# Kernel optimization log

Measured on AMD Instinct MI355X. Metric: run time of the kernel, lower is better.

Reference implementation:

```python
import jax, jax.numpy as jnp
import numpy as np

N, G, MAX_N, E, H = 20000, 200, 100, 320000, 4
F_IN, NHID, NCLS = 128, 128, 10
DQ = 2 * NHID   # pooling-stack input dim = 2*nhid
K1 = 25         # ceil(0.25 * avg_num_nodes)


def _lin(key, fi, fo):
    kw, kb = jax.random.split(key)
    s = 1.0 / np.sqrt(fi)
    return (jax.random.uniform(kw, (fi, fo), jnp.float32, -s, s),
            jax.random.uniform(kb, (fo,), jnp.float32, -s, s))


def setup_inputs():
    key = jax.random.key(0)
    ks = jax.random.split(key, 32)
    x = jax.random.normal(ks[0], (N, F_IN), jnp.float32)
    gid = jax.random.randint(ks[1], (E,), 0, G)
    u = jax.random.randint(ks[2], (E,), 0, MAX_N)
    v = jax.random.randint(ks[3], (E,), 0, MAX_N)
    edge_index = jnp.stack([gid * MAX_N + u, gid * MAX_N + v]).astype(jnp.int32)
    batch = (jnp.arange(N) // MAX_N).astype(jnp.int32)
    d = {}
    d['x'], d['edge_index'], d['batch'] = x, edge_index, batch
    d['W1'], d['b1'] = _lin(ks[4], F_IN, NHID)
    d['W2'], d['b2'] = _lin(ks[5], NHID, NHID)
    d['S0'] = jax.random.normal(ks[6], (1, K1, DQ), jnp.float32) * (1.0 / np.sqrt(DQ))
    d['Wq0'], d['bq0'] = _lin(ks[7], DQ, DQ)
    d['Wk0'], d['bk0'] = _lin(ks[8], DQ, DQ)
    d['Wv0'], d['bv0'] = _lin(ks[9], DQ, DQ)
    d['Wo0'], d['bo0'] = _lin(ks[10], DQ, DQ)
    d['Wq1'], d['bq1'] = _lin(ks[11], DQ, NHID)
    d['Wk1'], d['bk1'] = _lin(ks[12], DQ, NHID)
    d['Wv1'], d['bv1'] = _lin(ks[13], DQ, NHID)
    d['Wo1'], d['bo1'] = _lin(ks[14], NHID, NHID)
    d['S2'] = jax.random.normal(ks[15], (1, 1, NHID), jnp.float32) * (1.0 / np.sqrt(NHID))
    d['Wq2'], d['bq2'] = _lin(ks[16], NHID, NHID)
    d['Wk2'], d['bk2'] = _lin(ks[17], NHID, NHID)
    d['Wv2'], d['bv2'] = _lin(ks[18], NHID, NHID)
    d['Wo2'], d['bo2'] = _lin(ks[19], NHID, NHID)
    d['Wl'], d['bl'] = _lin(ks[20], NHID, NHID)
    d['Wc1'], d['bc1'] = _lin(ks[21], NHID, NHID)
    d['Wc2'], d['bc2'] = _lin(ks[22], NHID, NHID // 2)
    d['Wc3'], d['bc3'] = _lin(ks[23], NHID // 2, NCLS)
    return d


def gcn(h, src, dst, W, b):
    # PyG GCNConv: add self loops, sym-normalize, scatter-add, bias
    h = h @ W
    loop = jnp.arange(N, dtype=src.dtype)
    s = jnp.concatenate([src, loop])
    t = jnp.concatenate([dst, loop])
    deg = jax.ops.segment_sum(jnp.ones(s.shape[0], h.dtype), t, num_segments=N)
    dinv = jax.lax.rsqrt(jnp.maximum(deg, 1.0))
    norm = (dinv[s] * dinv[t])[:, None]
    return jax.ops.segment_sum(h[s] * norm, t, num_segments=N) + b


def to_dense(v, batch):
    counts = jax.ops.segment_sum(jnp.ones(v.shape[0], jnp.int32), batch, num_segments=G)
    start = jnp.cumsum(counts) - counts
    pos = jnp.arange(v.shape[0]) - start[batch]
    dense = jnp.zeros((G, MAX_N, v.shape[1]), v.dtype).at[batch, pos].set(v)
    mask = jnp.zeros((G, MAX_N), bool).at[batch, pos].set(True)
    return dense, mask


def attn_block(Q, K, V, Wo, bo, mask_bias):
    # MAB core with cluster=True: softmax over the QUERY (seed) axis, ln=False
    B, nq, dv = Q.shape
    dh = dv // H
    Qh = Q.reshape(B, nq, H, dh)
    Kh = K.reshape(B, K.shape[1], H, dh)
    Vh = V.reshape(B, V.shape[1], H, dh)
    score = jnp.einsum('bqhd,bkhd->bhqk', Qh, Kh) / jnp.sqrt(jnp.float32(dv))
    if mask_bias is not None:
        score = score + mask_bias[:, None, None, :]
    A = jax.nn.softmax(score, axis=2)  # cluster assignment over seeds
    O = Q + jnp.einsum('bhqk,bkhd->bqhd', A, Vh).reshape(B, nq, dv)
    return O + jax.nn.relu(O @ Wo + bo)


def reference(x, edge_index, batch, W1, b1, W2, b2, S0, Wq0, bq0, Wk0, bk0, Wv0, bv0, Wo0, bo0,
              Wq1, bq1, Wk1, bk1, Wv1, bv1, Wo1, bo1, S2, Wq2, bq2, Wk2, bk2, Wv2, bv2, Wo2, bo2,
              Wl, bl, Wc1, bc1, Wc2, bc2, Wc3, bc3):
    src, dst = edge_index[0], edge_index[1]
    x1 = jax.nn.relu(gcn(x, src, dst, W1, b1))
    x2 = jax.nn.relu(gcn(x1, src, dst, W2, b2))
    p1 = jax.ops.segment_sum(x1, batch, num_segments=G)  # global_add_pool
    p2 = jax.ops.segment_sum(x2, batch, num_segments=G)
    xcat = jnp.concatenate([x1, x2], axis=1)             # [N, 2*nhid]
    dense, mask = to_dense(xcat, batch)
    mask_bias = (1.0 - mask.astype(jnp.float32)) * -1e9
    # --- GMPool_G: PMA with GCNConv for K/V on the node graph ---
    Kd, _ = to_dense(gcn(xcat, src, dst, Wk0, bk0), batch)
    Vd, _ = to_dense(gcn(xcat, src, dst, Wv0, bv0), batch)
    Q0 = jnp.broadcast_to(S0, (G, K1, DQ)) @ Wq0 + bq0
    O0 = attn_block(Q0, Kd, Vd, Wo0, bo0, mask_bias)     # [G, 25, 256]
    # --- SelfAtt (SAB), mask consumed above ---
    Q1 = O0 @ Wq1 + bq1
    K1d = O0 @ Wk1 + bk1
    V1d = O0 @ Wv1 + bv1
    O1 = attn_block(Q1, K1d, V1d, Wo1, bo1, None)        # [G, 25, 128]
    # --- GMPool_I: PMA with 1 seed ---
    Q2 = jnp.broadcast_to(S2, (G, 1, NHID)) @ Wq2 + bq2
    K2d = O1 @ Wk2 + bk2
    V2d = O1 @ Wv2 + bv2
    O2 = attn_block(Q2, K2d, V2d, Wo2, bo2, None)        # [G, 1, 128]
    z = (O2 @ Wl + bl)[:, 0, :]
    z = jax.nn.relu(z @ Wc1 + bc1)                        # dropout = identity at eval
    z = jax.nn.relu(z @ Wc2 + bc2)
    logits = z @ Wc3 + bc3
    return (logits, p1, p2)
```

## Files before the change

kernel.cpp:

```cpp
#include <hip/hip_runtime.h>
#include <hip/hip_bf16.h>
#include <cstdint>
#include <cstddef>

typedef __hip_bfloat16 bf16;
typedef __attribute__((ext_vector_type(8))) short s16x8;
typedef __attribute__((ext_vector_type(4))) float f32x4;

#define MAXN 100
#define HH   4
#define FIN  128
#define KS1  25
#define GLDK 136

static inline int ceil_div(int a, int b){ return (a + b - 1) / b; }

__device__ inline short f2bf(float f){
  unsigned int u = __float_as_uint(f);
  u = (u + 0x7FFF + ((u >> 16) & 1)) >> 16;
  return (short)u;
}
__device__ inline float loadf(const void* s, size_t i, bool isbf){
  return isbf ? __bfloat162float(((const bf16*)s)[i]) : ((const float*)s)[i];
}
__device__ inline bool block_sniff(const void* x, int tid, int* flagS){
  if (tid < 64){
    unsigned short b = ((const unsigned short*)x)[2 * tid];
    float v = __uint_as_float(((unsigned)b) << 16);
    float a = fabsf(v);
    bool ok = (a >= 6.1e-5f && a <= 16384.f);
    unsigned long long m = __ballot(ok);
    if (tid == 0) *flagS = (__popcll(m) >= 32) ? 1 : 0;
  }
  __syncthreads();
  return *flagS != 0;
}

struct PrepBatch {
  const void* src[40];
  void*       dst[40];
  int         a[40];
  int         b[40];
  int         blk0[41];
  int         ne;
  const void* xptr;
};

__global__ __launch_bounds__(256) void prep_all(PrepBatch pb){
  __shared__ int flagS;
  int tid = threadIdx.x;
  bool isbf = block_sniff(pb.xptr, tid, &flagS);
  int blk = blockIdx.x;
  int t = 0;
  while (t + 1 < pb.ne && pb.blk0[t + 1] <= blk) t++;
  int local = blk - pb.blk0[t];
  const void* s = pb.src[t];
  int bt = pb.b[t];
  if (bt < 0){
    float val = (bt == -2) ? 1.0f : 0.0f;
    int n = pb.a[t];
    float* d = (float*)pb.dst[t];
    int v = local * 256 + tid;
    int base = v * 4;
    if (base + 3 < n) ((float4*)d)[v] = make_float4(val, val, val, val);
    else for (int j = base; j < n && j < base + 4; j++) d[j] = val;
  } else if (bt == 0){
    int n = pb.a[t];
    float* d = (float*)pb.dst[t];
    int v = local * 256 + tid;
    int base = v * 4;
    if (base + 3 < n){
      float4 f;
      if (isbf){
        ushort4 u = ((const ushort4*)s)[v];
        f.x = __uint_as_float(((unsigned)u.x) << 16);
        f.y = __uint_as_float(((unsigned)u.y) << 16);
        f.z = __uint_as_float(((unsigned)u.z) << 16);
        f.w = __uint_as_float(((unsigned)u.w) << 16);
      } else f = ((const float4*)s)[v];
      ((float4*)d)[v] = f;
    } else {
      for (int j = base; j < n && j < base + 4; j++) d[j] = loadf(s, j, isbf);
    }
  } else {
    int K = pb.a[t], Nn = bt, ldt = K + 8;
    short* d = (short*)pb.dst[t];
    int i = local * 256 + tid;
    if (i < K * Nn){
      int n = i / K, k = i - n * K;
      d[(size_t)n * ldt + k] = f2bf(loadf(s, (size_t)k * Nn + n, isbf));
    }
  }
}

__global__ __launch_bounds__(256) void adj_cnt(const int* __restrict__ src, const int* __restrict__ dst,
                                               float* __restrict__ A, int e){
  int i = blockIdx.x * 256 + threadIdx.x;
  if (i >= e) return;
  int s = src[i], d = dst[i];
  int g = d / MAXN;
  int dl = d - g * MAXN;
  int sl = s - (s / MAXN) * MAXN;
  atomicAdd(&A[(size_t)g * (MAXN * MAXN) + dl * MAXN + sl], 1.0f);
}

__global__ __launch_bounds__(256) void ubar_q0(const float* __restrict__ S0,
    const float* __restrict__ Wq0, const float* __restrict__ bq0,
    const float* __restrict__ Wk0, const float* __restrict__ bk0,
    float* __restrict__ Q0, short* __restrict__ Ubart, float* __restrict__ cvec)
{
  __shared__ float q0s[64];
  int j = blockIdx.x, h = j / 25, q = j - h * 25;
  int tid = threadIdx.x;
  if (tid < 64){
    int c = h * 64 + tid;
    float acc = bq0[c];
    for (int e = 0; e < 256; e++) acc = fmaf(S0[q * 256 + e], Wq0[e * 256 + c], acc);
    q0s[tid] = acc;
    Q0[q * 256 + c] = acc;
  }
  __syncthreads();
  float acc = 0.f;
  const float* wp = &Wk0[(size_t)tid * 256 + h * 64];
#pragma unroll
  for (int d = 0; d < 64; d++) acc = fmaf(wp[d], q0s[d], acc);
  Ubart[(size_t)j * 264 + tid] = f2bf(acc * 0.0625f);
  if (tid == 0){
    float cb = 0.f;
    for (int d = 0; d < 64; d++) cb = fmaf(bk0[h * 64 + d], q0s[d], cb);
    cvec[j] = cb * 0.0625f;
  }
}

struct GTParams {
  const void* X;
  const float* Adj;
  const short* W1t; const float* b1;
  const short* W2t; const float* b2;
  float* p1; float* p2;
  const short* Wv0t;
  const short* Ubart;
  const float* biasVS;
  const float* Q0;
  const short* Wo0t;  const float* bo0;
  const short* WQKVt; const float* biasQKV;
  const short* Wo1t;  const float* bo1;
  const float *S2w, *Wq2, *bq2, *Wv2, *bv2, *Wo2, *bo2, *Wl, *bl, *Wc1, *bc1, *Wc2, *bc2, *Wc3, *bc3;
  float* out;
};

__global__ __launch_bounds__(512) void gcn_tail(GTParams P)
{
  __shared__ __align__(16) char pool[162880];
  __shared__ float dinvL[112];
  __shared__ int flagS;
  short* S1x = (short*)(pool);
  short* S2b = (short*)(pool + 30464);
  short* S4b = (short*)(pool + 65280);
  short* Asb = (short*)(pool + 100096);
  char* R1 = pool;
  char* RV = pool + 57344;
  char* RS = pool + 122880;
  float* Ssh  = (float*)RS;
  short* Pbf  = (short*)R1;
  short* Abf  = (short*)(R1 + 34816);
  float* hva  = (float*)(R1 + 51712);
  float* hvb  = (float*)(R1 + 52224);
  float* O1F  = (float*)R1;
  float* OaF  = (float*)RS;
  float* ObF  = (float*)RS;
  short* Abf2 = (short*)(RS + 26000);
  float* QKV  = (float*)RV;
  float* Ss2  = (float*)(RV + 38800);
  float* hpart= (float*)(RV + 38800);

  int g = blockIdx.x, tid = threadIdx.x;
  bool isbf = block_sniff(P.X, tid, &flagS);
  int wave = tid >> 6, lane = tid & 63, quad = lane >> 4, l16 = lane & 15;
  int gn = wave * 16 + l16;

  for (int i = tid; i < 162880 / 4; i += 512) ((int*)pool)[i] = 0;

  const float* Ag = P.Adj + (size_t)g * (MAXN * MAXN);
  if (tid < 400){
    int r = tid >> 2, j0 = (tid & 3) * 25;
    const float* row = Ag + r * MAXN + j0;
    float s = 0.f;
#pragma unroll
    for (int j = 0; j < 25; j++) s += row[j];
    s += __shfl_xor(s, 1); s += __shfl_xor(s, 2);
    if ((tid & 3) == 0) dinvL[r] = rsqrtf(1.0f + s);
  }
  __syncthreads();

  for (int i = tid; i < MAXN * MAXN; i += 512){
    int r = i / MAXN, s = i - r * MAXN;
    float v = Ag[i] + (r == s ? 1.0f : 0.0f);
    Asb[r * GLDK + s] = f2bf(v * dinvL[r] * dinvL[s]);
  }
  for (int i = tid; i < MAXN * 16; i += 512){
    int r = i >> 4, k8 = (i & 15) << 3;
    s16x8 v;
    if (isbf){
      v = *reinterpret_cast<const s16x8*>((const short*)P.X + (size_t)(g * MAXN + r) * 128 + k8);
    } else {
      const float* ap = (const float*)P.X + (size_t)(g * MAXN + r) * 128 + k8;
      float4 f0 = *reinterpret_cast<const float4*>(ap);
      float4 f1 = *reinterpret_cast<const float4*>(ap + 4);
      v[0] = f2bf(f0.x); v[1] = f2bf(f0.y); v[2] = f2bf(f0.z); v[3] = f2bf(f0.w);
      v[4] = f2bf(f1.x); v[5] = f2bf(f1.y); v[6] = f2bf(f1.z); v[7] = f2bf(f1.w);
    }
    *reinterpret_cast<s16x8*>(&S1x[r * GLDK + k8]) = v;
  }
  __syncthreads();

  f32x4 acc[7];
  auto zacc = [&](){
#pragma unroll
    for (int rt = 0; rt < 7; rt++) acc[rt] = (f32x4){0.f,0.f,0.f,0.f};
  };
  auto passL = [&](const short* Abuf, const short* Bbuf){
#pragma unroll
    for (int kt = 0; kt < 4; kt++){
      int kb = kt * 32 + quad * 8;
      s16x8 bf0 = *reinterpret_cast<const s16x8*>(&Bbuf[gn * GLDK + kb]);
#pragma unroll
      for (int rt = 0; rt < 7; rt++){
        s16x8 a = *reinterpret_cast<const s16x8*>(&Abuf[(rt * 16 + l16) * GLDK + kb]);
        acc[rt] = __builtin_amdgcn_mfma_f32_16x16x32_bf16(a, bf0, acc[rt], 0, 0, 0);
      }
    }
  };
  auto passG = [&](const short* Abuf, const short* __restrict__ Bt){
#pragma unroll
    for (int kt = 0; kt < 4; kt++){
      int kb = kt * 32 + quad * 8;
      s16x8 bf0 = *reinterpret_cast<const s16x8*>(&Bt[(size_t)gn * 136 + kb]);
#pragma unroll
      for (int rt = 0; rt < 7; rt++){
        s16x8 a = *reinterpret_cast<const s16x8*>(&Abuf[(rt * 16 + l16) * GLDK + kb]);
        acc[rt] = __builtin_amdgcn_mfma_f32_16x16x32_bf16(a, bf0, acc[rt], 0, 0, 0);
      }
    }
  };
  auto writeB = [&](short* Bbuf){
#pragma unroll
    for (int rt = 0; rt < 7; rt++){
      short4 o;
      o.x = f2bf(acc[rt][0]); o.y = f2bf(acc[rt][1]);
      o.z = f2bf(acc[rt][2]); o.w = f2bf(acc[rt][3]);
      *reinterpret_cast<short4*>(&Bbuf[gn * GLDK + rt * 16 + quad * 4]) = o;
    }
  };
  float s1sum = 0.f, s2sum = 0.f;
  auto hopEpi = [&](const float* bias, short* AoutA, short* BoutB, float& sum){
    float bv = bias[gn];
#pragma unroll
    for (int rt = 0; rt < 7; rt++){
      float vals[4];
#pragma unroll
      for (int r = 0; r < 4; r++){
        int row = rt * 16 + quad * 4 + r;
        float v = fmaxf(acc[rt][r] + bv, 0.f);
        vals[r] = v;
        if (row < MAXN) sum += v;
      }
      short4 o;
      o.x = f2bf(vals[0]); o.y = f2bf(vals[1]); o.z = f2bf(vals[2]); o.w = f2bf(vals[3]);
      *reinterpret_cast<short4*>(&BoutB[gn * GLDK + rt * 16 + quad * 4]) = o;
      if (AoutA){
        AoutA[(rt * 16 + quad * 4 + 0) * GLDK + gn] = o.x;
        AoutA[(rt * 16 + quad * 4 + 1) * GLDK + gn] = o.y;
        AoutA[(rt * 16 + quad * 4 + 2) * GLDK + gn] = o.z;
        AoutA[(rt * 16 + quad * 4 + 3) * GLDK + gn] = o.w;
      }
    }
  };

  zacc(); passG(S1x, P.W1t); writeB(S2b);
  __syncthreads();
  zacc(); passL(Asb, S2b); hopEpi(P.b1, S1x, S4b, s1sum);
  __syncthreads();
  short4 xag0[7];
  zacc(); passL(Asb, S4b);
#pragma unroll
  for (int rt = 0; rt < 7; rt++){
    xag0[rt].x = f2bf(acc[rt][0]); xag0[rt].y = f2bf(acc[rt][1]);
    xag0[rt].z = f2bf(acc[rt][2]); xag0[rt].w = f2bf(acc[rt][3]);
  }
  zacc(); passG(S1x, P.W2t); writeB(S2b);
  __syncthreads();
  zacc(); passL(Asb, S2b); hopEpi(P.b2, nullptr, S4b, s2sum);
  __syncthreads();
  zacc(); passL(Asb, S4b);

  s1sum += __shfl_xor(s1sum, 16); s1sum += __shfl_xor(s1sum, 32);
  s2sum += __shfl_xor(s2sum, 16); s2sum += __shfl_xor(s2sum, 32);
  if (quad == 0){
    P.p1[g * 128 + gn] = s1sum;
    P.p2[g * 128 + gn] = s2sum;
  }
  __syncthreads();

  {
    short v0[4];
#pragma unroll
    for (int rt = 0; rt < 7; rt++){
      v0[0] = xag0[rt].x; v0[1] = xag0[rt].y; v0[2] = xag0[rt].z; v0[3] = xag0[rt].w;
#pragma unroll
      for (int r = 0; r < 4; r++){
        int node = rt * 16 + quad * 4 + r;
        if (node < MAXN){
          int sw = (node & 7) << 4;
          *(short*)(R1 + ((node * 512 + gn * 2) ^ sw)) = v0[r];
          *(short*)(R1 + ((node * 512 + (gn + 128) * 2) ^ sw)) = f2bf(acc[rt][r]);
        }
      }
    }
    for (int i = tid; i < 1536; i += 512) ((int*)(R1 + 51200))[i] = 0;
  }
  __syncthreads();

  {
#pragma unroll
    for (int cg = 0; cg < 2; cg++){
      int c = wave * 32 + cg * 16 + l16;
      const short* bw = P.Wv0t + (size_t)c * 264;
      s16x8 B[8];
#pragma unroll
      for (int kt = 0; kt < 8; kt++) B[kt] = *reinterpret_cast<const s16x8*>(bw + kt * 32 + quad * 8);
      f32x4 vac[7];
#pragma unroll
      for (int rt = 0; rt < 7; rt++) vac[rt] = (f32x4){0.f,0.f,0.f,0.f};
#pragma unroll
      for (int kt = 0; kt < 8; kt++){
        int kb = kt * 32 + quad * 8;
#pragma unroll
        for (int rt = 0; rt < 7; rt++){
          int row = rt * 16 + l16;
          int ab = (row * 512 + kb * 2) ^ ((row & 7) << 4);
          s16x8 a = *reinterpret_cast<const s16x8*>(R1 + ab);
          vac[rt] = __builtin_amdgcn_mfma_f32_16x16x32_bf16(a, B[kt], vac[rt], 0, 0, 0);
        }
      }
      float bv = P.biasVS[c];
#pragma unroll
      for (int rt = 0; rt < 7; rt++){
        int node0 = rt * 16 + quad * 4;
        short4 o;
        o.x = f2bf(vac[rt][0] + bv); o.y = f2bf(vac[rt][1] + bv);
        o.z = f2bf(vac[rt][2] + bv); o.w = f2bf(vac[rt][3] + bv);
        int b = (c * 256 + node0 * 2) ^ ((c & 7) << 4);
        *reinterpret_cast<short4*>(RV + b) = o;
      }
    }
    if (wave < 7){
      int j = wave * 16 + l16;
      const short* bw = P.Ubart + (size_t)j * 264;
      s16x8 B[8];
#pragma unroll
      for (int kt = 0; kt < 8; kt++) B[kt] = *reinterpret_cast<const s16x8*>(bw + kt * 32 + quad * 8);
      f32x4 sac[7];
#pragma unroll
      for (int rt = 0; rt < 7; rt++) sac[rt] = (f32x4){0.f,0.f,0.f,0.f};
#pragma unroll
      for (int kt = 0; kt < 8; kt++){
        int kb = kt * 32 + quad * 8;
#pragma unroll
        for (int rt = 0; rt < 7; rt++){
          int row = rt * 16 + l16;
          int ab = (row * 512 + kb * 2) ^ ((row & 7) << 4);
          s16x8 a = *reinterpret_cast<const s16x8*>(R1 + ab);
          sac[rt] = __builtin_amdgcn_mfma_f32_16x16x32_bf16(a, B[kt], sac[rt], 0, 0, 0);
        }
      }
      if (j < 100){
        float cv = P.biasVS[256 + j];
#pragma unroll
        for (int rt = 0; rt < 7; rt++){
#pragma unroll
          for (int r = 0; r < 4; r++){
            int node = rt * 16 + quad * 4 + r;
            if (node < MAXN) Ssh[node * 100 + j] = sac[rt][r] + cv;
          }
        }
      }
    }
  }
  __syncthreads();

  if (tid < 400){
    int k = tid >> 2, h = tid & 3;
    const float* base = &Ssh[k * 100 + h * 25];
    float v[25];
    float m = -1e30f;
#pragma unroll
    for (int q = 0; q < 25; q++){ v[q] = base[q]; m = fmaxf(m, v[q]); }
    float s = 0.f;
#pragma unroll
    for (int q = 0; q < 25; q++){ float e = __expf(v[q] - m); v[q] = e; s += e; }
    float inv = 1.0f / s;
    short* pb = &Pbf[h * 32 * 136 + k];
#pragma unroll
    for (int q = 0; q < 25; q++) pb[q * 136] = f2bf(v[q] * inv);
  } else {
    for (int idx = tid - 400; idx < 1400; idx += 112){
      int r = idx / 14, c = idx - r * 14;
      int h = r / 25, q = r - h * 25;
      ((int*)Pbf)[(h * 32 + q) * 68 + 50 + c] = 0;
    }
  }
  __syncthreads();

  {
    int h = wave >> 1;
    int cbase = wave * 32;
    f32x4 aac[2][2];
#pragma unroll
    for (int rt = 0; rt < 2; rt++){ aac[rt][0] = (f32x4){0.f,0.f,0.f,0.f}; aac[rt][1] = aac[rt][0]; }
#pragma unroll
    for (int kt = 0; kt < 4; kt++){
      int kb = kt * 32 + quad * 8;
      int c0 = cbase + l16, c1 = cbase + 16 + l16;
      int b0 = (c0 * 256 + kb * 2) ^ ((c0 & 7) << 4);
      int b1 = (c1 * 256 + kb * 2) ^ ((c1 & 7) << 4);
      s16x8 vb0 = *reinterpret_cast<const s16x8*>(RV + b0);
      s16x8 vb1 = *reinterpret_cast<const s16x8*>(RV + b1);
#pragma unroll
      for (int rt = 0; rt < 2; rt++){
        s16x8 a = *reinterpret_cast<const s16x8*>(&Pbf[(h * 32 + rt * 16 + l16) * 136 + kb]);
        aac[rt][0] = __builtin_amdgcn_mfma_f32_16x16x32_bf16(a, vb0, aac[rt][0], 0, 0, 0);
        aac[rt][1] = __builtin_amdgcn_mfma_f32_16x16x32_bf16(a, vb1, aac[rt][1], 0, 0, 0);
      }
    }
#pragma unroll
    for (int cg = 0; cg < 2; cg++){
      int c = cbase + cg * 16 + l16;
#pragma unroll
      for (int rt = 0; rt < 2; rt++){
#pragma unroll
        for (int r = 0; r < 4; r++){
          int row = rt * 16 + quad * 4 + r;
          if (row < 25){
            float oa = aac[rt][cg][r] + P.Q0[row * 256 + c];
            OaF[row * 260 + c] = oa;
            Abf[row * 264 + c] = f2bf(oa);
          }
        }
      }
    }
  }
  __syncthreads();

  {
    int c0 = wave * 16 + l16, c1 = c0 + 128;
    s16x8 B0[8], B1[8];
#pragma unroll
    for (int kt = 0; kt < 8; kt++){
      int kb = kt * 32 + quad * 8;
      B0[kt] = *reinterpret_cast<const s16x8*>(&P.Wo0t[(size_t)c0 * 264 + kb]);
      B1[kt] = *reinterpret_cast<const s16x8*>(&P.Wo0t[(size_t)c1 * 264 + kb]);
    }
    f32x4 a0[2], a1[2];
#pragma unroll
    for (int rt = 0; rt < 2; rt++){ a0[rt] = (f32x4){0.f,0.f,0.f,0.f}; a1[rt] = a0[rt]; }
#pragma unroll
    for (int kt = 0; kt < 8; kt++){
      int kb = kt * 32 + quad * 8;
#pragma unroll
      for (int rt = 0; rt < 2; rt++){
        s16x8 a = *reinterpret_cast<const s16x8*>(&Abf[(rt * 16 + l16) * 264 + kb]);
        a0[rt] = __builtin_amdgcn_mfma_f32_16x16x32_bf16(a, B0[kt], a0[rt], 0, 0, 0);
        a1[rt] = __builtin_amdgcn_mfma_f32_16x16x32_bf16(a, B1[kt], a1[rt], 0, 0, 0);
      }
    }
    __syncthreads();
#pragma unroll
    for (int cg = 0; cg < 2; cg++){
      int col = cg ? c1 : c0;
      float bv = P.bo0[col];
#pragma unroll
      for (int rt = 0; rt < 2; rt++){
        f32x4 av = cg ? a1[rt] : a0[rt];
#pragma unroll
        for (int r = 0; r < 4; r++){
          int row = rt * 16 + quad * 4 + r;
          if (row < 25){
            float t = av[r] + bv;
            Abf[row * 264 + col] = f2bf(OaF[row * 260 + col] + fmaxf(t, 0.f));
          }
        }
      }
    }
  }
  __syncthreads();

  {
    int c0 = wave * 16 + l16;
    s16x8 B[3][8];
#pragma unroll
    for (int p2 = 0; p2 < 3; p2++)
#pragma unroll
      for (int kt = 0; kt < 8; kt++){
        int kb = kt * 32 + quad * 8;
        B[p2][kt] = *reinterpret_cast<const s16x8*>(&P.WQKVt[(size_t)(c0 + p2 * 128) * 264 + kb]);
      }
    f32x4 qac[3][2];
#pragma unroll
    for (int p2 = 0; p2 < 3; p2++)
#pragma unroll
      for (int rt = 0; rt < 2; rt++) qac[p2][rt] = (f32x4){0.f,0.f,0.f,0.f};
#pragma unroll
    for (int kt = 0; kt < 8; kt++){
      int kb = kt * 32 + quad * 8;
#pragma unroll
      for (int rt = 0; rt < 2; rt++){
        s16x8 a = *reinterpret_cast<const s16x8*>(&Abf[(rt * 16 + l16) * 264 + kb]);
#pragma unroll
        for (int p2 = 0; p2 < 3; p2++)
          qac[p2][rt] = __builtin_amdgcn_mfma_f32_16x16x32_bf16(a, B[p2][kt], qac[p2][rt], 0, 0, 0);
      }
    }
#pragma unroll
    for (int p2 = 0; p2 < 3; p2++){
      int col = c0 + p2 * 128;
      float bv = P.biasQKV[col];
#pragma unroll
      for (int rt = 0; rt < 2; rt++){
#pragma unroll
        for (int r = 0; r < 4; r++){
          int row = rt * 16 + quad * 4 + r;
          if (row < 25) QKV[row * 388 + col] = qac[p2][rt][r] + bv;
        }
      }
    }
  }
  __syncthreads();

  for (int idx = tid; idx < 2500; idx += 512){
    int h = idx / 625;
    int r = idx - h * 625;
    int q = r / 25, k = r - q * 25;
    const float* qp = &QKV[q * 388 + h * 32];
    const float* kp = &QKV[k * 388 + 128 + h * 32];
    float sac = 0.f;
#pragma unroll
    for (int d = 0; d < 32; d += 4){
      float4 a4 = *reinterpret_cast<const float4*>(&qp[d]);
      float4 b4 = *reinterpret_cast<const float4*>(&kp[d]);
      sac = fmaf(a4.x, b4.x, sac); sac = fmaf(a4.y, b4.y, sac);
      sac = fmaf(a4.z, b4.z, sac); sac = fmaf(a4.w, b4.w, sac);
    }
    Ss2[(h * 25 + q) * 26 + k] = sac * 0.0883883476f;
  }
  __syncthreads();
  if (tid < 100){
    int h = tid / 25, k = tid - h * 25;
    float m = -1e30f;
#pragma unroll
    for (int q = 0; q < 25; q++) m = fmaxf(m, Ss2[(h * 25 + q) * 26 + k]);
    float s = 0.f;
#pragma unroll
    for (int q = 0; q < 25; q++){ float e = __expf(Ss2[(h * 25 + q) * 26 + k] - m); Ss2[(h * 25 + q) * 26 + k] = e; s += e; }
    float inv = 1.0f / s;
#pragma unroll
    for (int q = 0; q < 25; q++) Ss2[(h * 25 + q) * 26 + k] *= inv;
  }
  __syncthreads();

  if (tid < 256){
    int qh = tid >> 7;
    int c = tid & 127, h = c >> 5;
    int q0 = qh * 13, nq = 13 - qh;
    float oac[13] = {};
    for (int k = 0; k < 25; k++){
      float v = QKV[k * 388 + 256 + c];
      for (int j = 0; j < nq; j++)
        oac[j] = fmaf(Ss2[(h * 25 + q0 + j) * 26 + k], v, oac[j]);
    }
    for (int j = 0; j < nq; j++){
      int q = q0 + j;
      float ob = QKV[q * 388 + c] + oac[j];
      ObF[q * 132 + c] = ob;
      Abf2[q * 136 + c] = f2bf(ob);
    }
  }
  __syncthreads();

  {
    int c0 = wave * 16 + l16;
    s16x8 B0[4];
#pragma unroll
    for (int kt = 0; kt < 4; kt++){
      int kb = kt * 32 + quad * 8;
      B0[kt] = *reinterpret_cast<const s16x8*>(&P.Wo1t[(size_t)c0 * 136 + kb]);
    }
    f32x4 a0 = (f32x4){0.f,0.f,0.f,0.f}, a1 = a0;
#pragma unroll
    for (int kt = 0; kt < 4; kt++){
      int kb = kt * 32 + quad * 8;
      s16x8 aA = *reinterpret_cast<const s16x8*>(&Abf2[l16 * 136 + kb]);
      s16x8 aB = *reinterpret_cast<const s16x8*>(&Abf2[(16 + l16) * 136 + kb]);
      a0 = __builtin_amdgcn_mfma_f32_16x16x32_bf16(aA, B0[kt], a0, 0, 0, 0);
      a1 = __builtin_amdgcn_mfma_f32_16x16x32_bf16(aB, B0[kt], a1, 0, 0, 0);
    }
    float bv = P.bo1[c0];
#pragma unroll
    for (int r = 0; r < 4; r++){
      int row0 = quad * 4 + r;
      if (row0 < 25){ float t = a0[r] + bv; O1F[row0 * 132 + c0] = ObF[row0 * 132 + c0] + fmaxf(t, 0.f); }
      int row1 = 16 + quad * 4 + r;
      if (row1 < 25){ float t = a1[r] + bv; O1F[row1 * 132 + c0] = ObF[row1 * 132 + c0] + fmaxf(t, 0.f); }
    }
  }
  __syncthreads();

  if (tid < 128){
    float s = 0.f;
    for (int k = 0; k < 25; k++) s += O1F[k * 132 + tid];
    hva[tid] = s;
  }
  __syncthreads();
  {
    int kh = tid >> 7, c = tid & 127, k0 = kh * 32;
    float s = 0.f;
    for (int k = k0; k < k0 + 32; k++)
      s = fmaf(P.S2w[k], P.Wq2[k * 128 + c], fmaf(hva[k], P.Wv2[k * 128 + c], s));
    hpart[kh * 128 + c] = s;
    __syncthreads();
    if (tid < 128) hvb[c] = hpart[c] + hpart[128 + c] + hpart[256 + c] + hpart[384 + c]
                          + P.bq2[c] + 25.f * P.bv2[c];
    __syncthreads();
    s = 0.f;
    for (int k = k0; k < k0 + 32; k++) s = fmaf(hvb[k], P.Wo2[k * 128 + c], s);
    hpart[kh * 128 + c] = s;
    __syncthreads();
    if (tid < 128) hva[c] = hvb[c] + fmaxf(hpart[c] + hpart[128 + c] + hpart[256 + c] + hpart[384 + c] + P.bo2[c], 0.f);
    __syncthreads();
    s = 0.f;
    for (int k = k0; k < k0 + 32; k++) s = fmaf(hva[k], P.Wl[k * 128 + c], s);
    hpart[kh * 128 + c] = s;
    __syncthreads();
    if (tid < 128) hvb[c] = hpart[c] + hpart[128 + c] + hpart[256 + c] + hpart[384 + c] + P.bl[c];
    __syncthreads();
    s = 0.f;
    for (int k = k0; k < k0 + 32; k++) s = fmaf(hvb[k], P.Wc1[k * 128 + c], s);
    hpart[kh * 128 + c] = s;
    __syncthreads();
    if (tid < 128) hva[c] = fmaxf(hpart[c] + hpart[128 + c] + hpart[256 + c] + hpart[384 + c] + P.bc1[c], 0.f);
    __syncthreads();
    {
      int kh2 = tid >> 6, c2 = tid & 63, kk0 = kh2 * 16;
      float s2 = 0.f;
      for (int k = kk0; k < kk0 + 16; k++) s2 = fmaf(hva[k], P.Wc2[k * 64 + c2], s2);
      hpart[kh2 * 64 + c2] = s2;
    }
    __syncthreads();
    if (tid < 64){
      float s2 = hpart[tid] + hpart[64 + tid] + hpart[128 + tid] + hpart[192 + tid]
               + hpart[256 + tid] + hpart[320 + tid] + hpart[384 + tid] + hpart[448 + tid];
      hvb[tid] = fmaxf(s2 + P.bc2[tid], 0.f);
    }
    __syncthreads();
    if (tid < 10){
      float lg = P.bc3[tid];
      for (int k = 0; k < 64; k++) lg = fmaf(hvb[k], P.Wc3[k * 10 + tid], lg);
      P.out[g * 10 + tid] = lg;
    }
  }
}

extern "C" void kernel_launch(void* const* d_in, const int* in_sizes, int n_in,
                              void* d_out, int out_size, void* d_ws, size_t ws_size,
                              hipStream_t stream)
{
  const int*  edge = (const int*)d_in[1];
  const int N = in_sizes[0] / FIN;
  const int E = in_sizes[1] / 2;
  const int G = N / MAXN;
  const int* srcp = edge;
  const int* dstp = edge + E;
  float* out = (float*)d_out;

  float* w = (float*)d_ws;
  size_t off = 0;
  auto alloc = [&](size_t nfl){ nfl = (nfl + 3) & ~(size_t)3; float* p = w + off; off += nfl; return p; };
  auto allocS = [&](size_t nsh)->short*{ size_t nfl = ((nsh + 1) / 2 + 3) & ~(size_t)3; short* p = (short*)(w + off); off += nfl; return p; };

  float* biasVS  = alloc(356);
  float* biasQKV = alloc(384);
  float* cvec = biasVS + 256;

  const int castT[24] = {4,6,7,8,9,10,11,15,23,24,25,26,29,30,31,32,33,34,35,36,37,38,39,40};
  float* wf[41] = {nullptr};
  for (int i = 0; i < 24; i++) wf[castT[i]] = alloc((size_t)in_sizes[castT[i]]);
  wf[13] = biasVS; wf[17] = biasQKV; wf[19] = biasQKV + 128; wf[21] = biasQKV + 256;

  float* Adj = alloc((size_t)G * MAXN * MAXN);
  float* Q0  = alloc(25 * 256);

  short* W1t   = allocS(128 * 136);
  short* W2t   = allocS(128 * 136);
  short* WVSt  = allocS(356 * 264);
  short* WQKVt = allocS(384 * 264);
  short* Wo0t  = allocS(256 * 264);
  short* Wo1t  = allocS(128 * 136);
  short* Ubart = WVSt + (size_t)256 * 264;
  if (off * sizeof(float) > ws_size) return;

  dim3 blk(256);

  PrepBatch pb; int ne = 0, blks = 0;
  pb.xptr = d_in[0];
  auto addC = [&](const void* s, float* d, int n){
    pb.src[ne]=s; pb.dst[ne]=d; pb.a[ne]=n; pb.b[ne]=0; pb.blk0[ne]=blks;
    blks += ceil_div(ceil_div(n, 4), 256); ne++; };
  auto addW = [&](const void* s, short* d, int K, int Nn){
    pb.src[ne]=s; pb.dst[ne]=d; pb.a[ne]=K; pb.b[ne]=Nn; pb.blk0[ne]=blks;
    blks += ceil_div(K * Nn, 256); ne++; };
  auto addF = [&](void* d, int n, int mode){
    pb.src[ne]=nullptr; pb.dst[ne]=d; pb.a[ne]=n; pb.b[ne]=mode; pb.blk0[ne]=blks;
    blks += ceil_div(ceil_div(n, 4), 256); ne++; };
  for (int i = 0; i < 24; i++){ int t = castT[i]; addC(d_in[t], wf[t], in_sizes[t]); }
  addC(d_in[13], biasVS, 256);
  addC(d_in[17], biasQKV, 128); addC(d_in[19], biasQKV + 128, 128); addC(d_in[21], biasQKV + 256, 128);
  addW(d_in[3],  W1t, 128, 128);             addW(d_in[5],  W2t, 128, 128);
  addW(d_in[12], WVSt, 256, 256);            addW(d_in[16], WQKVt, 256, 128);
  addW(d_in[18], WQKVt + 128*264, 256, 128); addW(d_in[20], WQKVt + 256*264, 256, 128);
  addW(d_in[14], Wo0t, 256, 256);            addW(d_in[22], Wo1t, 128, 128);
  addF(Adj, G * MAXN * MAXN, -1);
  pb.blk0[ne] = blks; pb.ne = ne;
  prep_all<<<dim3(blks), blk, 0, stream>>>(pb);

  adj_cnt<<<ceil_div(E, 256), blk, 0, stream>>>(srcp, dstp, Adj, E);

  ubar_q0<<<dim3(100), blk, 0, stream>>>(wf[7], wf[8], wf[9], wf[10], wf[11], Q0, Ubart, cvec);

  GTParams tp;
  tp.X = d_in[0]; tp.Adj = Adj;
  tp.W1t = W1t; tp.b1 = wf[4]; tp.W2t = W2t; tp.b2 = wf[6];
  tp.p1 = out + 2000; tp.p2 = out + 27600;
  tp.Wv0t = WVSt; tp.Ubart = Ubart; tp.biasVS = biasVS;
  tp.Q0 = Q0;
  tp.Wo0t = Wo0t; tp.bo0 = wf[15];
  tp.WQKVt = WQKVt; tp.biasQKV = biasQKV;
  tp.Wo1t = Wo1t; tp.bo1 = wf[23];
  tp.S2w = wf[24]; tp.Wq2 = wf[25]; tp.bq2 = wf[26]; tp.Wv2 = wf[29]; tp.bv2 = wf[30];
  tp.Wo2 = wf[31]; tp.bo2 = wf[32]; tp.Wl = wf[33]; tp.bl = wf[34];
  tp.Wc1 = wf[35]; tp.bc1 = wf[36]; tp.Wc2 = wf[37]; tp.bc2 = wf[38];
  tp.Wc3 = wf[39]; tp.bc3 = wf[40];
  tp.out = out;
  gcn_tail<<<dim3(G), dim3(512), 0, stream>>>(tp);
}
```

Before: 239.4 us.

## Prefetch weight fragments into registers ahead of barriers and stage adjacency in LDS

Global loads of weight fragments (W1, W2, Wv0, Ubar, Wo0, WQKV, Wo1) are issued into registers earlier, before the preceding barrier or compute, so their latency overlaps other work. The adjacency block is copied into shared memory with vector loads before degree and normalization are computed. The Q0 projection in the small precompute kernel is split across all 256 threads and its Wk0 dot product is vectorized. The cost is much higher register pressure in a 512-thread kernel, which may cause spills.

```diff
diff --git a/kernel.cpp b/kernel.cpp
--- a/kernel.cpp
+++ b/kernel.cpp
@@ -109,13 +109,23 @@
     const float* __restrict__ Wk0, const float* __restrict__ bk0,
     float* __restrict__ Q0, short* __restrict__ Ubart, float* __restrict__ cvec)
 {
+  __shared__ float part[256];
   __shared__ float q0s[64];
   int j = blockIdx.x, h = j / 25, q = j - h * 25;
   int tid = threadIdx.x;
+  {
+    int c = tid & 63, kq = tid >> 6;
+    const float* s0 = S0 + q * 256 + kq * 64;
+    const float* wq = Wq0 + (size_t)(kq * 64) * 256 + h * 64 + c;
+    float a = 0.f;
+#pragma unroll
+    for (int e = 0; e < 64; e++) a = fmaf(s0[e], wq[(size_t)e * 256], a);
+    part[kq * 64 + c] = a;
+  }
+  __syncthreads();
   if (tid < 64){
     int c = h * 64 + tid;
-    float acc = bq0[c];
-    for (int e = 0; e < 256; e++) acc = fmaf(S0[q * 256 + e], Wq0[e * 256 + c], acc);
+    float acc = bq0[c] + part[tid] + part[64 + tid] + part[128 + tid] + part[192 + tid];
     q0s[tid] = acc;
     Q0[q * 256 + c] = acc;
   }
@@ -123,7 +133,12 @@
   float acc = 0.f;
   const float* wp = &Wk0[(size_t)tid * 256 + h * 64];
 #pragma unroll
-  for (int d = 0; d < 64; d++) acc = fmaf(wp[d], q0s[d], acc);
+  for (int d = 0; d < 64; d += 4){
+    float4 w4 = *reinterpret_cast<const float4*>(wp + d);
+    float4 q4 = *reinterpret_cast<const float4*>(&q0s[d]);
+    acc = fmaf(w4.x, q4.x, acc); acc = fmaf(w4.y, q4.y, acc);
+    acc = fmaf(w4.z, q4.z, acc); acc = fmaf(w4.w, q4.w, acc);
+  }
   Ubart[(size_t)j * 264 + tid] = f2bf(acc * 0.0625f);
   if (tid == 0){
     float cb = 0.f;
@@ -158,6 +173,7 @@
   short* S2b = (short*)(pool + 30464);
   short* S4b = (short*)(pool + 65280);
   short* Asb = (short*)(pool + 100096);
+  float* AdjL = (float*)(pool + 30464);
   char* R1 = pool;
   char* RV = pool + 57344;
   char* RS = pool + 122880;
@@ -179,24 +195,21 @@
   int wave = tid >> 6, lane = tid & 63, quad = lane >> 4, l16 = lane & 15;
   int gn = wave * 16 + l16;
 
+  s16x8 w1f[4], w2f[4];
+#pragma unroll
+  for (int kt = 0; kt < 4; kt++){
+    int kb = kt * 32 + quad * 8;
+    w1f[kt] = *reinterpret_cast<const s16x8*>(P.W1t + (size_t)gn * 136 + kb);
+    w2f[kt] = *reinterpret_cast<const s16x8*>(P.W2t + (size_t)gn * 136 + kb);
+  }
+
   for (int i = tid; i < 162880 / 4; i += 512) ((int*)pool)[i] = 0;
-
-  const float* Ag = P.Adj + (size_t)g * (MAXN * MAXN);
-  if (tid < 400){
-    int r = tid >> 2, j0 = (tid & 3) * 25;
-    const float* row = Ag + r * MAXN + j0;
-    float s = 0.f;
-#pragma unroll
-    for (int j = 0; j < 25; j++) s += row[j];
-    s += __shfl_xor(s, 1); s += __shfl_xor(s, 2);
-    if ((tid & 3) == 0) dinvL[r] = rsqrtf(1.0f + s);
-  }
-  __syncthreads();
-
-  for (int i = tid; i < MAXN * MAXN; i += 512){
-    int r = i / MAXN, s = i - r * MAXN;
-    float v = Ag[i] + (r == s ? 1.0f : 0.0f);
-    Asb[r * GLDK + s] = f2bf(v * dinvL[r] * dinvL[s]);
+  __syncthreads();
+
+  {
+    const float* Ag = P.Adj + (size_t)g * (MAXN * MAXN);
+    for (int i = tid; i < 2500; i += 512)
+      ((float4*)AdjL)[i] = ((const float4*)Ag)[i];
   }
   for (int i = tid; i < MAXN * 16; i += 512){
     int r = i >> 4, k8 = (i & 15) << 3;
@@ -214,6 +227,24 @@
   }
   __syncthreads();
 
+  if (tid < 400){
+    int r = tid >> 2, j0 = (tid & 3) * 25;
+    const float* row = AdjL + r * 100 + j0;
+    float s = 0.f;
+#pragma unroll
+    for (int j = 0; j < 25; j++) s += row[j];
+    s += __shfl_xor(s, 1); s += __shfl_xor(s, 2);
+    if ((tid & 3) == 0) dinvL[r] = rsqrtf(1.0f + s);
+  }
+  __syncthreads();
+
+  for (int i = tid; i < MAXN * MAXN; i += 512){
+    int r = i / MAXN, s = i - r * MAXN;
+    float v = AdjL[i] + (r == s ? 1.0f : 0.0f);
+    Asb[r * GLDK + s] = f2bf(v * dinvL[r] * dinvL[s]);
+  }
+  __syncthreads();
+
   f32x4 acc[7];
   auto zacc = [&](){
 #pragma unroll
@@ -231,15 +262,14 @@
       }
     }
   };
-  auto passG = [&](const short* Abuf, const short* __restrict__ Bt){
+  auto passGF = [&](const short* Abuf, const s16x8* bfr){
 #pragma unroll
     for (int kt = 0; kt < 4; kt++){
       int kb = kt * 32 + quad * 8;
-      s16x8 bf0 = *reinterpret_cast<const s16x8*>(&Bt[(size_t)gn * 136 + kb]);
 #pragma unroll
       for (int rt = 0; rt < 7; rt++){
         s16x8 a = *reinterpret_cast<const s16x8*>(&Abuf[(rt * 16 + l16) * GLDK + kb]);
-        acc[rt] = __builtin_amdgcn_mfma_f32_16x16x32_bf16(a, bf0, acc[rt], 0, 0, 0);
+        acc[rt] = __builtin_amdgcn_mfma_f32_16x16x32_bf16(a, bfr[kt], acc[rt], 0, 0, 0);
       }
     }
   };
@@ -277,7 +307,7 @@
     }
   };
 
-  zacc(); passG(S1x, P.W1t); writeB(S2b);
+  zacc(); passGF(S1x, w1f); writeB(S2b);
   __syncthreads();
   zacc(); passL(Asb, S2b); hopEpi(P.b1, S1x, S4b, s1sum);
   __syncthreads();
@@ -288,11 +318,26 @@
     xag0[rt].x = f2bf(acc[rt][0]); xag0[rt].y = f2bf(acc[rt][1]);
     xag0[rt].z = f2bf(acc[rt][2]); xag0[rt].w = f2bf(acc[rt][3]);
   }
-  zacc(); passG(S1x, P.W2t); writeB(S2b);
+  zacc(); passGF(S1x, w2f); writeB(S2b);
   __syncthreads();
   zacc(); passL(Asb, S2b); hopEpi(P.b2, nullptr, S4b, s2sum);
   __syncthreads();
   zacc(); passL(Asb, S4b);
+
+  s16x8 wvf[2][8], ubf[8];
+  {
+#pragma unroll
+    for (int cg = 0; cg < 2; cg++){
+      int c = wave * 32 + cg * 16 + l16;
+      const short* bw = P.Wv0t + (size_t)c * 264;
+#pragma unroll
+      for (int kt = 0; kt < 8; kt++) wvf[cg][kt] = *reinterpret_cast<const s16x8*>(bw + kt * 32 + quad * 8);
+    }
+    int jj = (wave < 7) ? (wave * 16 + l16) : l16;
+    const short* bw = P.Ubart + (size_t)jj * 264;
+#pragma unroll
+    for (int kt = 0; kt < 8; kt++) ubf[kt] = *reinterpret_cast<const s16x8*>(bw + kt * 32 + quad * 8);
+  }
 
   s1sum += __shfl_xor(s1sum, 16); s1sum += __shfl_xor(s1sum, 32);
   s2sum += __shfl_xor(s2sum, 16); s2sum += __shfl_xor(s2sum, 32);
@@ -325,10 +370,6 @@
 #pragma unroll
     for (int cg = 0; cg < 2; cg++){
       int c = wave * 32 + cg * 16 + l16;
-      const short* bw = P.Wv0t + (size_t)c * 264;
-      s16x8 B[8];
-#pragma unroll
-      for (int kt = 0; kt < 8; kt++) B[kt] = *reinterpret_cast<const s16x8*>(bw + kt * 32 + quad * 8);
       f32x4 vac[7];
 #pragma unroll
       for (int rt = 0; rt < 7; rt++) vac[rt] = (f32x4){0.f,0.f,0.f,0.f};
@@ -340,7 +381,7 @@
           int row = rt * 16 + l16;
           int ab = (row * 512 + kb * 2) ^ ((row & 7) << 4);
           s16x8 a = *reinterpret_cast<const s16x8*>(R1 + ab);
-          vac[rt] = __builtin_amdgcn_mfma_f32_16x16x32_bf16(a, B[kt], vac[rt], 0, 0, 0);
+          vac[rt] = __builtin_amdgcn_mfma_f32_16x16x32_bf16(a, wvf[cg][kt], vac[rt], 0, 0, 0);
         }
       }
       float bv = P.biasVS[c];
@@ -356,10 +397,6 @@
     }
     if (wave < 7){
       int j = wave * 16 + l16;
-      const short* bw = P.Ubart + (size_t)j * 264;
-      s16x8 B[8];
-#pragma unroll
-      for (int kt = 0; kt < 8; kt++) B[kt] = *reinterpret_cast<const s16x8*>(bw + kt * 32 + quad * 8);
       f32x4 sac[7];
 #pragma unroll
       for (int rt = 0; rt < 7; rt++) sac[rt] = (f32x4){0.f,0.f,0.f,0.f};
@@ -371,7 +408,7 @@
           int row = rt * 16 + l16;
           int ab = (row * 512 + kb * 2) ^ ((row & 7) << 4);
           s16x8 a = *reinterpret_cast<const s16x8*>(R1 + ab);
-          sac[rt] = __builtin_amdgcn_mfma_f32_16x16x32_bf16(a, B[kt], sac[rt], 0, 0, 0);
+          sac[rt] = __builtin_amdgcn_mfma_f32_16x16x32_bf16(a, ubf[kt], sac[rt], 0, 0, 0);
         }
       }
       if (j < 100){
@@ -431,6 +468,16 @@
         s16x8 a = *reinterpret_cast<const s16x8*>(&Pbf[(h * 32 + rt * 16 + l16) * 136 + kb]);
         aac[rt][0] = __builtin_amdgcn_mfma_f32_16x16x32_bf16(a, vb0, aac[rt][0], 0, 0, 0);
         aac[rt][1] = __builtin_amdgcn_mfma_f32_16x16x32_bf16(a, vb1, aac[rt][1], 0, 0, 0);
+      }
+    }
+    s16x8 o0f0[8], o0f1[8];
+    {
+      int c0w = wave * 16 + l16, c1w = c0w + 128;
+#pragma unroll
+      for (int kt = 0; kt < 8; kt++){
+        int kb = kt * 32 + quad * 8;
+        o0f0[kt] = *reinterpret_cast<const s16x8*>(&P.Wo0t[(size_t)c0w * 264 + kb]);
+        o0f1[kt] = *reinterpret_cast<const s16x8*>(&P.Wo0t[(size_t)c1w * 264 + kb]);
       }
     }
 #pragma unroll
@@ -449,76 +496,72 @@
         }
       }
     }
-  }
-  __syncthreads();
-
-  {
-    int c0 = wave * 16 + l16, c1 = c0 + 128;
-    s16x8 B0[8], B1[8];
+    __syncthreads();
+
+    {
+      int c0 = wave * 16 + l16, c1 = c0 + 128;
+      f32x4 a0[2], a1[2];
+#pragma unroll
+      for (int rt = 0; rt < 2; rt++){ a0[rt] = (f32x4){0.f,0.f,0.f,0.f}; a1[rt] = a0[rt]; }
+#pragma unroll
+      for (int kt = 0; kt < 8; kt++){
+        int kb = kt * 32 + quad * 8;
+#pragma unroll
+        for (int rt = 0; rt < 2; rt++){
+          s16x8 a = *reinterpret_cast<const s16x8*>(&Abf[(rt * 16 + l16) * 264 + kb]);
+          a0[rt] = __builtin_amdgcn_mfma_f32_16x16x32_bf16(a, o0f0[kt], a0[rt], 0, 0, 0);
+          a1[rt] = __builtin_amdgcn_mfma_f32_16x16x32_bf16(a, o0f1[kt], a1[rt], 0, 0, 0);
+        }
+      }
+      __syncthreads();
+#pragma unroll
+      for (int cg = 0; cg < 2; cg++){
+        int col = cg ? c1 : c0;
+        float bv = P.bo0[col];
+#pragma unroll
+        for (int rt = 0; rt < 2; rt++){
+          f32x4 av = cg ? a1[rt] : a0[rt];
+#pragma unroll
+          for (int r = 0; r < 4; r++){
+            int row = rt * 16 + quad * 4 + r;
+            if (row < 25){
+              float t = av[r] + bv;
+              Abf[row * 264 + col] = f2bf(OaF[row * 260 + col] + fmaxf(t, 0.f));
+            }
+          }
+        }
+      }
+    }
+  }
+  s16x8 qkvf[3][8];
+  {
+    int c0 = wave * 16 + l16;
+#pragma unroll
+    for (int p2 = 0; p2 < 3; p2++)
+#pragma unroll
+      for (int kt = 0; kt < 8; kt++){
+        int kb = kt * 32 + quad * 8;
+        qkvf[p2][kt] = *reinterpret_cast<const s16x8*>(&P.WQKVt[(size_t)(c0 + p2 * 128) * 264 + kb]);
+      }
+  }
+  __syncthreads();
+
+  {
+    int c0 = wave * 16 + l16;
+    f32x4 qac[3][2];
+#pragma unroll
+    for (int p2 = 0; p2 < 3; p2++)
+#pragma unroll
+      for (int rt = 0; rt < 2; rt++) qac[p2][rt] = (f32x4){0.f,0.f,0.f,0.f};
 #pragma unroll
     for (int kt = 0; kt < 8; kt++){
       int kb = kt * 32 + quad * 8;
-      B0[kt] = *reinterpret_cast<const s16x8*>(&P.Wo0t[(size_t)c0 * 264 + kb]);
-      B1[kt] = *reinterpret_cast<const s16x8*>(&P.Wo0t[(size_t)c1 * 264 + kb]);
-    }
-    f32x4 a0[2], a1[2];
-#pragma unroll
-    for (int rt = 0; rt < 2; rt++){ a0[rt] = (f32x4){0.f,0.f,0.f,0.f}; a1[rt] = a0[rt]; }
-#pragma unroll
-    for (int kt = 0; kt < 8; kt++){
-      int kb = kt * 32 + quad * 8;
 #pragma unroll
       for (int rt = 0; rt < 2; rt++){
         s16x8 a = *reinterpret_cast<const s16x8*>(&Abf[(rt * 16 + l16) * 264 + kb]);
-        a0[rt] = __builtin_amdgcn_mfma_f32_16x16x32_bf16(a, B0[kt], a0[rt], 0, 0, 0);
-        a1[rt] = __builtin_amdgcn_mfma_f32_16x16x32_bf16(a, B1[kt], a1[rt], 0, 0, 0);
-      }
-    }
-    __syncthreads();
-#pragma unroll
-    for (int cg = 0; cg < 2; cg++){
-      int col = cg ? c1 : c0;
-      float bv = P.bo0[col];
-#pragma unroll
-      for (int rt = 0; rt < 2; rt++){
-        f32x4 av = cg ? a1[rt] : a0[rt];
-#pragma unroll
-        for (int r = 0; r < 4; r++){
-          int row = rt * 16 + quad * 4 + r;
-          if (row < 25){
-            float t = av[r] + bv;
-            Abf[row * 264 + col] = f2bf(OaF[row * 260 + col] + fmaxf(t, 0.f));
-          }
-        }
-      }
-    }
-  }
-  __syncthreads();
-
-  {
-    int c0 = wave * 16 + l16;
-    s16x8 B[3][8];
-#pragma unroll
-    for (int p2 = 0; p2 < 3; p2++)
-#pragma unroll
-      for (int kt = 0; kt < 8; kt++){
-        int kb = kt * 32 + quad * 8;
-        B[p2][kt] = *reinterpret_cast<const s16x8*>(&P.WQKVt[(size_t)(c0 + p2 * 128) * 264 + kb]);
-      }
-    f32x4 qac[3][2];
-#pragma unroll
-    for (int p2 = 0; p2 < 3; p2++)
-#pragma unroll
-      for (int rt = 0; rt < 2; rt++) qac[p2][rt] = (f32x4){0.f,0.f,0.f,0.f};
-#pragma unroll
-    for (int kt = 0; kt < 8; kt++){
-      int kb = kt * 32 + quad * 8;
-#pragma unroll
-      for (int rt = 0; rt < 2; rt++){
-        s16x8 a = *reinterpret_cast<const s16x8*>(&Abf[(rt * 16 + l16) * 264 + kb]);
 #pragma unroll
         for (int p2 = 0; p2 < 3; p2++)
-          qac[p2][rt] = __builtin_amdgcn_mfma_f32_16x16x32_bf16(a, B[p2][kt], qac[p2][rt], 0, 0, 0);
+          qac[p2][rt] = __builtin_amdgcn_mfma_f32_16x16x32_bf16(a, qkvf[p2][kt], qac[p2][rt], 0, 0, 0);
       }
     }
 #pragma unroll
@@ -585,24 +628,27 @@
       Abf2[q * 136 + c] = f2bf(ob);
     }
   }
-  __syncthreads();
-
+  s16x8 o1f[4];
   {
     int c0 = wave * 16 + l16;
-    s16x8 B0[4];
 #pragma unroll
     for (int kt = 0; kt < 4; kt++){
       int kb = kt * 32 + quad * 8;
-      B0[kt] = *reinterpret_cast<const s16x8*>(&P.Wo1t[(size_t)c0 * 136 + kb]);
-    }
+      o1f[kt] = *reinterpret_cast<const s16x8*>(&P.Wo1t[(size_t)c0 * 136 + kb]);
+    }
+  }
+  __syncthreads();
+
+  {
+    int c0 = wave * 16 + l16;
     f32x4 a0 = (f32x4){0.f,0.f,0.f,0.f}, a1 = a0;
 #pragma unroll
     for (int kt = 0; kt < 4; kt++){
       int kb = kt * 32 + quad * 8;
       s16x8 aA = *reinterpret_cast<const s16x8*>(&Abf2[l16 * 136 + kb]);
       s16x8 aB = *reinterpret_cast<const s16x8*>(&Abf2[(16 + l16) * 136 + kb]);
-      a0 = __builtin_amdgcn_mfma_f32_16x16x32_bf16(aA, B0[kt], a0, 0, 0, 0);
-      a1 = __builtin_amdgcn_mfma_f32_16x16x32_bf16(aB, B0[kt], a1, 0, 0, 0);
+      a0 = __builtin_amdgcn_mfma_f32_16x16x32_bf16(aA, o1f[kt], a0, 0, 0, 0);
+      a1 = __builtin_amdgcn_mfma_f32_16x16x32_bf16(aB, o1f[kt], a1, 0, 0, 0);
     }
     float bv = P.bo1[c0];
 #pragma unroll
```

Result: faster. 230.6 us (-3.7%).
